# Optimization experiments

Hardware: AMD Instinct MI355X
Metric: run time of the kernel (lower is better)

Reference implementation:

```python
import jax, jax.numpy as jnp
import numpy as np


def _ln(x, w, b):
    m = x.mean(-1, keepdims=True)
    v = ((x - m) ** 2).mean(-1, keepdims=True)
    return (x - m) * jax.lax.rsqrt(v + 1e-5) * w + b


def _l2n(x):
    return x / jnp.clip(jnp.linalg.norm(x, axis=-1, keepdims=True), 1e-12, None)


def _forward(tokens, emb, ln1_w, ln1_b, wq, wkv, wo, wo_b, knn_scale,
             ln2_w, ln2_b, ff_w1, ff_b1, ff_w2, ff_b2, lnf_w, lnf_b,
             w_logits, b_logits, xl_mems, db_kv, knn_layer, topk):
    B, N = tokens.shape
    depth = wq.shape[0]
    H = knn_scale.shape[0]
    Dh = wkv.shape[-1] // 2
    XL = xl_mems.shape[2]
    NEG = jnp.finfo(emb.dtype).max
    x = emb[tokens]  # [B,N,dim]
    # causal mask with XL-cache offset: triu(j - i + 1)
    causal = jnp.triu(jnp.ones((N, N + XL), bool), XL + 1)
    for l in range(depth):
        h = _ln(x, ln1_w[l], ln1_b[l])
        q = (h @ wq[l]).reshape(B, N, H, Dh).transpose(0, 2, 1, 3)  # [B,H,N,Dh]
        kv = h @ wkv[l]
        k, v = kv[..., :Dh], kv[..., Dh:]  # single shared kv head [B,N,Dh]
        is_knn = (l == knn_layer)
        if is_knn:
            q, k = _l2n(q), _l2n(k)
            scale = jnp.exp(knn_scale)[None, :, None, None]
        else:
            q = q * (Dh ** -0.5)
            scale = 1.0
        k = jnp.concatenate((xl_mems[l, :, :, 0], k), axis=1)  # [B,N+XL,Dh]
        v = jnp.concatenate((xl_mems[l, :, :, 1], v), axis=1)
        sim = jnp.einsum('bhid,bjd->bhij', q, k) * scale
        sim = jnp.where(causal, -NEG, sim)
        if is_knn:
            dbk = _l2n(db_kv[..., 0, :])  # [B,M,Dh] stored keys are l2-normalized
            dbv = db_kv[..., 1, :]
            simdb = jnp.einsum('bhid,bmd->bhim', q, dbk)
            _, idx = jax.lax.top_k(simdb, topk)  # [B,H,N,topk] inner-product KNN
            mem_k = jax.vmap(lambda t, i: t[i])(dbk, idx)  # [B,H,N,topk,Dh]
            mem_v = jax.vmap(lambda t, i: t[i])(dbv, idx)
            sim_mem = jnp.einsum('bhid,bhijd->bhij', q, mem_k) * scale
            attn = jax.nn.softmax(jnp.concatenate((sim_mem, sim), axis=-1), axis=-1)
            mem_attn, loc_attn = attn[..., :topk], attn[..., topk:]
            out = (jnp.einsum('bhij,bjd->bhid', loc_attn, v)
                   + jnp.einsum('bhij,bhijd->bhid', mem_attn, mem_v))
        else:
            attn = jax.nn.softmax(sim, axis=-1)
            out = jnp.einsum('bhij,bjd->bhid', attn, v)
        out = out.transpose(0, 2, 1, 3).reshape(B, N, H * Dh)
        x = out @ wo[l] + wo_b[l] + x
        h = _ln(x, ln2_w[l], ln2_b[l])
        x = jax.nn.gelu(h @ ff_w1[l] + ff_b1[l], approximate=False) @ ff_w2[l] + ff_b2[l] + x
    return _ln(x, lnf_w, lnf_b) @ w_logits + b_logits


def setup_inputs() -> dict:
    B, N, DIM, H, DH, DEPTH, V, XL, M = 2, 1024, 1024, 16, 64, 4, 32000, 256, 4096
    key = jax.random.key(0)
    ks = jax.random.split(key, 12)
    s = 0.02
    rn = lambda k, sh: (jax.random.normal(k, sh) * s).astype(jnp.float32)
    return dict(
        tokens=jax.random.randint(ks[0], (B, N), 0, V, dtype=jnp.int32),
        emb=rn(ks[1], (V, DIM)),
        ln1_w=jnp.ones((DEPTH, DIM), jnp.float32), ln1_b=jnp.zeros((DEPTH, DIM), jnp.float32),
        wq=rn(ks[2], (DEPTH, DIM, H * DH)),
        wkv=rn(ks[3], (DEPTH, DIM, 2 * DH)),
        wo=rn(ks[4], (DEPTH, H * DH, DIM)), wo_b=jnp.zeros((DEPTH, DIM), jnp.float32),
        knn_scale=jnp.full((H,), float(np.log(20.0)), jnp.float32),
        ln2_w=jnp.ones((DEPTH, DIM), jnp.float32), ln2_b=jnp.zeros((DEPTH, DIM), jnp.float32),
        ff_w1=rn(ks[5], (DEPTH, DIM, 4 * DIM)), ff_b1=jnp.zeros((DEPTH, 4 * DIM), jnp.float32),
        ff_w2=rn(ks[6], (DEPTH, 4 * DIM, DIM)), ff_b2=jnp.zeros((DEPTH, DIM), jnp.float32),
        lnf_w=jnp.ones((DIM,), jnp.float32), lnf_b=jnp.zeros((DIM,), jnp.float32),
        w_logits=rn(ks[7], (DIM, V)), b_logits=jnp.zeros((V,), jnp.float32),
        xl_mems=jax.random.normal(ks[8], (DEPTH, B, XL, 2, DH), jnp.float32),
        db_kv=jax.random.normal(ks[9], (B, M, 2, DH), jnp.float32),
        knn_layer=2, topk=32,
    )


def reference(tokens, emb, ln1_w, ln1_b, wq, wkv, wo, wo_b, knn_scale,
              ln2_w, ln2_b, ff_w1, ff_b1, ff_w2, ff_b2, lnf_w, lnf_b,
              w_logits, b_logits, xl_mems, db_kv, knn_layer, topk):
    return _forward(tokens, emb, ln1_w, ln1_b, wq, wkv, wo, wo_b, knn_scale,
                    ln2_w, ln2_b, ff_w1, ff_b1, ff_w2, ff_b2, lnf_w, lnf_b,
                    w_logits, b_logits, xl_mems, db_kv, knn_layer, topk)
```

## Files before the change

### kernel.cpp

```cpp
#include <hip/hip_runtime.h>
#include <hip/hip_bf16.h>
#include <math.h>

#define BB 2
#define NSEQ 1024
#define DIM 1024
#define NH 16
#define DH 64
#define DEPTH 4
#define VOCAB 32000
#define XLM 256
#define MDB 4096
#define TOPK 32
#define KNN_LAYER 2
#define BNROWS (BB * NSEQ)
#define LOGITS_CHUNK 6400
#define NKEYS 1280
#define NQKV 1152
#define KSP_PS ((size_t)BB * NKEYS * DH)

typedef __bf16 bf16x8v __attribute__((ext_vector_type(8)));
typedef float f32x4v __attribute__((ext_vector_type(4)));
typedef unsigned short u16x8v __attribute__((ext_vector_type(8)));

__device__ __forceinline__ float bfbits2f(unsigned short u) {
    union { float f; unsigned int i; } v; v.i = ((unsigned int)u) << 16; return v.f;
}
__device__ __forceinline__ unsigned short f2bfbits(float f) {
    union { __hip_bfloat16 b; unsigned short u; } v;
    v.b = __float2bfloat16(f);
    return v.u;
}
__device__ __forceinline__ float bf2f(__hip_bfloat16 h) { return __bfloat162float(h); }
__device__ __forceinline__ __hip_bfloat16 f2bf(float f) { return __float2bfloat16(f); }

__device__ __forceinline__ void gload16(const void* gp, void* lp) {
    __builtin_amdgcn_global_load_lds(
        (const __attribute__((address_space(1))) unsigned int*)gp,
        (__attribute__((address_space(3))) unsigned int*)lp, 16, 0, 0);
}

__global__ __launch_bounds__(256) void embed_kernel(const int* __restrict__ tok,
                                                    const float* __restrict__ emb,
                                                    float* __restrict__ x) {
    int r = blockIdx.x, t = threadIdx.x;
    int id = tok[r];
    const float* er = emb + (size_t)id * DIM;
    float* xr = x + (size_t)r * DIM;
#pragma unroll
    for (int i = 0; i < 4; i++) xr[t + 256 * i] = er[t + 256 * i];
}

__global__ __launch_bounds__(256) void ln_kernel(const float* __restrict__ x,
                                                 const float* __restrict__ w,
                                                 const float* __restrict__ b,
                                                 __hip_bfloat16* __restrict__ y,
                                                 size_t ypS) {
    __shared__ float red[256];
    int r = blockIdx.x, t = threadIdx.x;
    const float* xr = x + (size_t)r * DIM;
    float v[4];
#pragma unroll
    for (int i = 0; i < 4; i++) v[i] = xr[t + 256 * i];
    float s = v[0] + v[1] + v[2] + v[3];
    red[t] = s; __syncthreads();
    for (int st = 128; st; st >>= 1) { if (t < st) red[t] += red[t + st]; __syncthreads(); }
    float mean = red[0] * (1.0f / DIM);
    __syncthreads();
    float s2 = 0.f;
#pragma unroll
    for (int i = 0; i < 4; i++) { float d = v[i] - mean; s2 += d * d; }
    red[t] = s2; __syncthreads();
    for (int st = 128; st; st >>= 1) { if (t < st) red[t] += red[t + st]; __syncthreads(); }
    float rs = rsqrtf(red[0] * (1.0f / DIM) + 1e-5f);
    __hip_bfloat16* yr = y + (size_t)r * DIM;
#pragma unroll
    for (int i = 0; i < 4; i++) {
        int c = t + 256 * i;
        float val = (v[i] - mean) * rs * w[c] + b[c];
        __hip_bfloat16 hv = f2bf(val);
        yr[c] = hv;
        yr[c + ypS] = f2bf(val - bf2f(hv));
    }
}

template <int NP>
__global__ __launch_bounds__(256) void combine_ln(const float* __restrict__ pbuf, size_t pS,
                                                  const float* __restrict__ bias,
                                                  float* __restrict__ x,
                                                  const float* __restrict__ w,
                                                  const float* __restrict__ b,
                                                  __hip_bfloat16* __restrict__ y,
                                                  size_t ypS) {
    __shared__ float red[256];
    int r = blockIdx.x, t = threadIdx.x;
    float v[4];
#pragma unroll
    for (int i = 0; i < 4; i++) {
        int c = t + 256 * i;
        size_t idx = (size_t)r * DIM + c;
        float s = bias[c] + x[idx];
#pragma unroll
        for (int z = 0; z < NP; z++) s += pbuf[(size_t)z * pS + idx];
        v[i] = s;
        x[idx] = s;
    }
    float s = v[0] + v[1] + v[2] + v[3];
    red[t] = s; __syncthreads();
    for (int st = 128; st; st >>= 1) { if (t < st) red[t] += red[t + st]; __syncthreads(); }
    float mean = red[0] * (1.0f / DIM);
    __syncthreads();
    float s2 = 0.f;
#pragma unroll
    for (int i = 0; i < 4; i++) { float d = v[i] - mean; s2 += d * d; }
    red[t] = s2; __syncthreads();
    for (int st = 128; st; st >>= 1) { if (t < st) red[t] += red[t + st]; __syncthreads(); }
    float rs = rsqrtf(red[0] * (1.0f / DIM) + 1e-5f);
    __hip_bfloat16* yr = y + (size_t)r * DIM;
#pragma unroll
    for (int i = 0; i < 4; i++) {
        int c = t + 256 * i;
        float val = (v[i] - mean) * rs * w[c] + b[c];
        __hip_bfloat16 hv = f2bf(val);
        yr[c] = hv;
        yr[c + ypS] = f2bf(val - bf2f(hv));
    }
}

__global__ void l2split_q(float* __restrict__ qf, unsigned short* __restrict__ qs,
                          size_t pS) {
    int r = blockIdx.x, t = threadIdx.x;
    size_t idx = (size_t)r * DH + t;
    float v = qf[idx];
    float s = v * v;
#pragma unroll
    for (int off = 32; off; off >>= 1) s += __shfl_xor(s, off, 64);
    float n = fmaxf(sqrtf(s), 1e-12f);
    v /= n;
    qf[idx] = v;
    unsigned short hv = f2bfbits(v);
    qs[idx] = hv;
    qs[idx + pS] = f2bfbits(v - bfbits2f(hv));
}

__global__ void dbnorm_kernel(const float* __restrict__ db, float* __restrict__ dbkn) {
    int r = blockIdx.x, t = threadIdx.x;
    float v = db[((size_t)r * 2 + 0) * DH + t];
    float s = v * v;
#pragma unroll
    for (int off = 32; off; off >>= 1) s += __shfl_xor(s, off, 64);
    float n = fmaxf(sqrtf(s), 1e-12f);
    dbkn[(size_t)r * DH + t] = v / n;
}

__global__ __launch_bounds__(256) void split_conv(const float* __restrict__ x,
                                                  unsigned short* __restrict__ y,
                                                  size_t pS, size_t n4) {
    size_t idx = (size_t)blockIdx.x * 256 + threadIdx.x;
    if (idx >= n4) return;
    float4 v = *(const float4*)&x[idx * 4];
    float vv[4] = {v.x, v.y, v.z, v.w};
    ushort4 h4, l4;
    unsigned short* hp = (unsigned short*)&h4;
    unsigned short* lp = (unsigned short*)&l4;
#pragma unroll
    for (int j = 0; j < 4; j++) {
        hp[j] = f2bfbits(vv[j]);
        lp[j] = f2bfbits(vv[j] - bfbits2f(hp[j]));
    }
    *(ushort4*)&y[idx * 4] = h4;
    *(ushort4*)&y[idx * 4 + pS] = l4;
}

template <int NP>
__global__ __launch_bounds__(256) void combine_k(const float* __restrict__ pbuf, size_t pS,
                                                 float* __restrict__ out,
                                                 const float* __restrict__ bias,
                                                 const float* __restrict__ res,
                                                 int N, size_t n4) {
    size_t idx = (size_t)blockIdx.x * 256 + threadIdx.x;
    if (idx >= n4) return;
    f32x4v s = *(const f32x4v*)&pbuf[idx * 4];
#pragma unroll
    for (int z = 1; z < NP; z++) {
        f32x4v v = *(const f32x4v*)&pbuf[(size_t)z * pS + idx * 4];
        s += v;
    }
    if (bias) {
        int col = (int)((idx * 4) % (size_t)N);
        const f32x4v bv = *(const f32x4v*)&bias[col];
        s += bv;
    }
    if (res) {
        f32x4v r = *(const f32x4v*)&res[idx * 4];
        s += r;
    }
    *(f32x4v*)&out[idx * 4] = s;
}

template <int NP>
__global__ __launch_bounds__(256) void combine_qkv(const float* __restrict__ pbuf, size_t pS,
                                                   float* __restrict__ qf,
                                                   float* __restrict__ kvf,
                                                   size_t n4) {
    size_t idx = (size_t)blockIdx.x * 256 + threadIdx.x;
    if (idx >= n4) return;
    f32x4v s = *(const f32x4v*)&pbuf[idx * 4];
#pragma unroll
    for (int z = 1; z < NP; z++) {
        f32x4v v = *(const f32x4v*)&pbuf[(size_t)z * pS + idx * 4];
        s += v;
    }
    size_t e = idx * 4;
    size_t row = e / NQKV;
    int col = (int)(e - row * NQKV);
    if (col < DIM) *(f32x4v*)&qf[row * DIM + col] = s;
    else *(f32x4v*)&kvf[row * 128 + (col - DIM)] = s;
}

template <int NP>
__global__ __launch_bounds__(256) void combine_gelu_split(const float* __restrict__ pbuf, size_t pS,
                                                          const float* __restrict__ bias, int N,
                                                          unsigned short* __restrict__ y, size_t ypS,
                                                          size_t n4) {
    size_t idx = (size_t)blockIdx.x * 256 + threadIdx.x;
    if (idx >= n4) return;
    f32x4v s = *(const f32x4v*)&pbuf[idx * 4];
#pragma unroll
    for (int z = 1; z < NP; z++) {
        f32x4v v = *(const f32x4v*)&pbuf[(size_t)z * pS + idx * 4];
        s += v;
    }
    int col = (int)((idx * 4) % (size_t)N);
    const f32x4v bv = *(const f32x4v*)&bias[col];
    s += bv;
    ushort4 h4, l4;
    unsigned short* hp = (unsigned short*)&h4;
    unsigned short* lp = (unsigned short*)&l4;
#pragma unroll
    for (int j = 0; j < 4; j++) {
        float v = s[j];
        v = 0.5f * v * (1.0f + erff(v * 0.70710678118654752f));
        hp[j] = f2bfbits(v);
        lp[j] = f2bfbits(v - bfbits2f(hp[j]));
    }
    *(ushort4*)&y[idx * 4] = h4;
    *(ushort4*)&y[idx * 4 + ypS] = l4;
}

template <int NORM>
__global__ void kv_prep(const float* __restrict__ kvf, const float* __restrict__ xlm,
                        unsigned short* __restrict__ ksp, unsigned short* __restrict__ vtp) {
    int key = blockIdx.x, b = blockIdx.y, d = threadIdx.x;
    float kvv, vvv;
    if (key < XLM) {
        kvv = xlm[(((size_t)b * XLM + key) * 2 + 0) * DH + d];
        vvv = xlm[(((size_t)b * XLM + key) * 2 + 1) * DH + d];
    } else {
        const float* r = &kvf[(size_t)(b * NSEQ + key - XLM) * 128];
        kvv = r[d]; vvv = r[64 + d];
        if (NORM) {
            float s = kvv * kvv;
#pragma unroll
            for (int off = 32; off; off >>= 1) s += __shfl_xor(s, off, 64);
            kvv /= fmaxf(sqrtf(s), 1e-12f);
        }
    }
    unsigned short kh = f2bfbits(kvv), kl = f2bfbits(kvv - bfbits2f(kh));
    unsigned short vh = f2bfbits(vvv), vl = f2bfbits(vvv - bfbits2f(vh));
    size_t ko = (size_t)b * NKEYS * DH + (size_t)key * DH + d;
    ksp[ko] = kh; ksp[ko + KSP_PS] = kl;
    size_t vo = (size_t)b * DH * NKEYS + (size_t)d * NKEYS + key;
    vtp[vo] = vh; vtp[vo + KSP_PS] = vl;
}

__global__ __launch_bounds__(256) void wconv(const float* __restrict__ W,
                                             __hip_bfloat16* __restrict__ WT,
                                             size_t wpS, int K, int N, int ldw,
                                             int wlo) {
    __shared__ float tile[64][65];
    int k0 = blockIdx.x * 64, n0 = blockIdx.y * 64;
    int t = threadIdx.x;
    int r = t >> 4, c4 = (t & 15) * 4;
#pragma unroll
    for (int rr = 0; rr < 4; rr++) {
        int row = rr * 16 + r;
        float4 v = *(const float4*)&W[(size_t)(k0 + row) * ldw + n0 + c4];
        tile[row][c4] = v.x; tile[row][c4 + 1] = v.y; tile[row][c4 + 2] = v.z; tile[row][c4 + 3] = v.w;
    }
    __syncthreads();
#pragma unroll
    for (int rr = 0; rr < 4; rr++) {
        int nrow = rr * 16 + r;
        size_t base = (size_t)(n0 + nrow) * K + k0 + c4;
#pragma unroll
        for (int j = 0; j < 4; j++) {
            float val = tile[c4 + j][nrow];
            __hip_bfloat16 hv = f2bf(val);
            WT[base + j] = hv;
            if (wlo) WT[base + j + wpS] = f2bf(val - bf2f(hv));
        }
    }
}

template <typename OT, int ACT, int TERMS, int MODE>
__global__ __launch_bounds__(256) void gemm_split(const __hip_bfloat16* __restrict__ A, int lda, size_t apS,
                                                  const __hip_bfloat16* __restrict__ BT, int ldb, size_t bpS,
                                                  OT* __restrict__ C, int ldc, size_t cpS, int K,
                                                  const float* __restrict__ bias,
                                                  const float* __restrict__ res,
                                                  int bh0) {
    __shared__ __align__(16) __hip_bfloat16 sAh[128 * 32];
    __shared__ __align__(16) __hip_bfloat16 sBh[128 * 32];
    __shared__ __align__(16) __hip_bfloat16 sAl[TERMS >= 2 ? 128 * 32 : 1];
    __shared__ __align__(16) __hip_bfloat16 sBl[TERMS >= 3 ? 128 * 32 : 1];
    if constexpr (MODE == 1) {
        int bh = bh0 + blockIdx.z;
        A += ((size_t)(bh >> 4) * NSEQ) * lda + (bh & 15) * DH;
        BT += (size_t)(bh >> 4) * MDB * ldb;
        C += (size_t)blockIdx.z * NSEQ * ldc;
    }
    if constexpr (MODE == 2) {
        A += (size_t)blockIdx.z * K;
        BT += (size_t)blockIdx.z * K;
        C += (size_t)blockIdx.z * cpS;
    }
    int bn = blockIdx.x * 128;
    int bm = blockIdx.y * 128;
    int t = threadIdx.x;
    int lane = t & 63, wid = t >> 6;
    int wr = wid >> 1, wc = wid & 1;
    int lr = lane & 15, kc = lane >> 4;

    f32x4v acc[4][4];
#pragma unroll
    for (int m = 0; m < 4; m++)
#pragma unroll
        for (int n = 0; n < 4; n++) acc[m][n] = (f32x4v){0.f, 0.f, 0.f, 0.f};

    for (int k0 = 0; k0 < K; k0 += 32) {
        __syncthreads();
#pragma unroll
        for (int it = 0; it < 2; it++) {
            int e = wid * 128 + it * 64 + lane;
            int r = e >> 2;
            int cl = (e & 3) ^ ((r >> 1) & 3);
            size_t aoff = (size_t)(bm + r) * lda + k0 + cl * 8;
            size_t boff = (size_t)(bn + r) * ldb + k0 + cl * 8;
            int dst = (wid * 128 + it * 64) * 8;
            gload16(&A[aoff], &sAh[dst]);
            gload16(&BT[boff], &sBh[dst]);
            if constexpr (TERMS >= 2) gload16(&A[aoff + apS], &sAl[dst]);
            if constexpr (TERMS >= 3) gload16(&BT[boff + bpS], &sBl[dst]);
        }
        __syncthreads();

        bf16x8v ah[4], al[4], bh[4], bl[4];
#pragma unroll
        for (int m = 0; m < 4; m++) {
            int row = wr * 64 + m * 16 + lr;
            int off = row * 32 + ((kc ^ ((row >> 1) & 3)) << 3);
            ah[m] = *(const bf16x8v*)&sAh[off];
            if constexpr (TERMS >= 2) al[m] = *(const bf16x8v*)&sAl[off];
        }
#pragma unroll
        for (int n = 0; n < 4; n++) {
            int row = wc * 64 + n * 16 + lr;
            int off = row * 32 + ((kc ^ ((row >> 1) & 3)) << 3);
            bh[n] = *(const bf16x8v*)&sBh[off];
            if constexpr (TERMS >= 3) bl[n] = *(const bf16x8v*)&sBl[off];
        }
#pragma unroll
        for (int m = 0; m < 4; m++)
#pragma unroll
            for (int n = 0; n < 4; n++) {
                acc[m][n] = __builtin_amdgcn_mfma_f32_16x16x32_bf16(ah[m], bh[n], acc[m][n], 0, 0, 0);
                if constexpr (TERMS >= 2)
                    acc[m][n] = __builtin_amdgcn_mfma_f32_16x16x32_bf16(al[m], bh[n], acc[m][n], 0, 0, 0);
                if constexpr (TERMS >= 3)
                    acc[m][n] = __builtin_amdgcn_mfma_f32_16x16x32_bf16(ah[m], bl[n], acc[m][n], 0, 0, 0);
            }
    }

#pragma unroll
    for (int m = 0; m < 4; m++) {
#pragma unroll
        for (int n = 0; n < 4; n++) {
            int gcol = bn + wc * 64 + n * 16 + lr;
            float bv = bias ? bias[gcol] : 0.f;
#pragma unroll
            for (int j = 0; j < 4; j++) {
                int grow = bm + wr * 64 + m * 16 + kc * 4 + j;
                float v = acc[m][n][j] + bv;
                if (ACT == 1) v = 0.5f * v * (1.0f + erff(v * 0.70710678118654752f));
                if (res) v += res[(size_t)grow * ldc + gcol];
                size_t idx = (size_t)grow * ldc + gcol;
                if constexpr (__is_same(OT, float)) {
                    C[idx] = v;
                } else if constexpr (__is_same(OT, unsigned short)) {
                    C[idx] = f2bfbits(v);
                } else {
                    __hip_bfloat16 hv = f2bf(v);
                    C[idx] = hv;
                    C[idx + cpS] = f2bf(v - bf2f(hv));
                }
            }
        }
    }
}

template <int KNNL>
__global__ __launch_bounds__(256) void flash_kernel(const float* __restrict__ q,
                                                    const unsigned short* __restrict__ ksp,
                                                    const unsigned short* __restrict__ vtp,
                                                    const float* __restrict__ knn_scale,
                                                    __hip_bfloat16* __restrict__ out,
                                                    size_t opS,
                                                    float* __restrict__ stats) {
    __shared__ __align__(16) unsigned short sKh[2][4096];
    __shared__ __align__(16) unsigned short sKl[2][4096];
    __shared__ __align__(16) unsigned short sVh[2][4096];
    __shared__ __align__(16) unsigned short sVl[2][4096];
    __shared__ __align__(16) float sPf[4 * 16 * 64];

    int qt = blockIdx.x, h = blockIdx.y, b = blockIdx.z;
    int q0 = qt * 64;
    int t = threadIdx.x;
    int w = t >> 6;
    int lane = t & 63;
    int lr = lane & 15, kc = lane >> 4;
    int wbase = w * 1024;

    float scale = KNNL ? __expf(knn_scale[h]) : 0.125f;

    bf16x8v qh[2], ql[2];
    {
        const float* qbase = q + (size_t)(b * NSEQ + q0 + w * 16 + lr) * DIM + h * DH;
#pragma unroll
        for (int ks = 0; ks < 2; ks++) {
            const float* s = qbase + ks * 32 + kc * 8;
            float4 a = *(const float4*)s;
            float4 c2 = *(const float4*)(s + 4);
            float vv[8] = {a.x, a.y, a.z, a.w, c2.x, c2.y, c2.z, c2.w};
            u16x8v hi, lo;
#pragma unroll
            for (int j = 0; j < 8; j++) {
                hi[j] = f2bfbits(vv[j]);
                lo[j] = f2bfbits(vv[j] - bfbits2f(hi[j]));
            }
            qh[ks] = *(bf16x8v*)&hi;
            ql[ks] = *(bf16x8v*)&lo;
        }
    }

    float m[4], l[4];
    f32x4v o[4];
#pragma unroll
    for (int j = 0; j < 4; j++) { m[j] = -1e30f; l[j] = 0.f; }
#pragma unroll
    for (int f = 0; f < 4; f++) o[f] = (f32x4v){0.f, 0.f, 0.f, 0.f};

    int ntiles = 5 + qt;
    size_t kbase = (size_t)b * NKEYS * DH;
    size_t vbase = (size_t)b * DH * NKEYS;

    auto stage = [&](int buf, int T) {
#pragma unroll
        for (int i2 = 0; i2 < 2; i2++) {
            int cbase = i2 * 256 + w * 64;
            int c = cbase + lane;
            int key = c >> 3, ch = (c & 7) ^ (key & 7);
            size_t ko = kbase + (size_t)(T * 64 + key) * DH + ch * 8;
            gload16(&ksp[ko], &sKh[buf][cbase * 8]);
            gload16(&ksp[ko + KSP_PS], &sKl[buf][cbase * 8]);
            int dim = c >> 3, k8 = (c & 7) ^ (dim & 7);
            size_t vo = vbase + (size_t)dim * NKEYS + T * 64 + k8 * 8;
            gload16(&vtp[vo], &sVh[buf][cbase * 8]);
            gload16(&vtp[vo + KSP_PS], &sVl[buf][cbase * 8]);
        }
    };

    stage(0, 0);
    __syncthreads();
    int cur = 0;

    for (int T = 0; T < ntiles; T++) {
        if (T + 1 < ntiles) stage(cur ^ 1, T + 1);

        f32x4v s4[4];
#pragma unroll
        for (int n = 0; n < 4; n++) s4[n] = (f32x4v){0.f, 0.f, 0.f, 0.f};
#pragma unroll
        for (int ks = 0; ks < 2; ks++) {
            bf16x8v qh_ = qh[ks], ql_ = ql[ks];
#pragma unroll
            for (int n = 0; n < 4; n++) {
                int row = n * 16 + lr;
                int off = row * 64 + (((ks * 4 + kc) ^ (lr & 7)) << 3);
                bf16x8v kh = *(const bf16x8v*)&sKh[cur][off];
                bf16x8v kl = *(const bf16x8v*)&sKl[cur][off];
                s4[n] = __builtin_amdgcn_mfma_f32_16x16x32_bf16(qh_, kh, s4[n], 0, 0, 0);
                s4[n] = __builtin_amdgcn_mfma_f32_16x16x32_bf16(ql_, kh, s4[n], 0, 0, 0);
                s4[n] = __builtin_amdgcn_mfma_f32_16x16x32_bf16(qh_, kl, s4[n], 0, 0, 0);
            }
        }

#pragma unroll
        for (int n = 0; n < 4; n++) {
            int key = T * 64 + n * 16 + lr;
#pragma unroll
            for (int j = 0; j < 4; j++) {
                int gq = q0 + w * 16 + kc * 4 + j;
                float sv = s4[n][j] * scale;
                s4[n][j] = (key <= XLM + gq) ? sv : -1e30f;
            }
        }

        float tm[4];
#pragma unroll
        for (int j = 0; j < 4; j++) {
            float v = fmaxf(fmaxf(s4[0][j], s4[1][j]), fmaxf(s4[2][j], s4[3][j]));
            v = fmaxf(v, __shfl_xor(v, 1, 64));
            v = fmaxf(v, __shfl_xor(v, 2, 64));
            v = fmaxf(v, __shfl_xor(v, 4, 64));
            v = fmaxf(v, __shfl_xor(v, 8, 64));
            tm[j] = v;
        }
        float alpha[4];
#pragma unroll
        for (int j = 0; j < 4; j++) {
            float mnew = fmaxf(m[j], tm[j]);
            alpha[j] = __expf(m[j] - mnew);
            m[j] = mnew;
        }
        float psum[4] = {0.f, 0.f, 0.f, 0.f};
#pragma unroll
        for (int n = 0; n < 4; n++)
#pragma unroll
            for (int j = 0; j < 4; j++) {
                float p = __expf(s4[n][j] - m[j]);
                s4[n][j] = p;
                psum[j] += p;
            }
#pragma unroll
        for (int j = 0; j < 4; j++) {
            float v = psum[j];
            v += __shfl_xor(v, 1, 64);
            v += __shfl_xor(v, 2, 64);
            v += __shfl_xor(v, 4, 64);
            v += __shfl_xor(v, 8, 64);
            l[j] = l[j] * alpha[j] + v;
        }
#pragma unroll
        for (int f = 0; f < 4; f++)
#pragma unroll
            for (int j = 0; j < 4; j++) o[f][j] *= alpha[j];

#pragma unroll
        for (int n = 0; n < 4; n++) {
            int chunkcol = 2 * n + (lr >> 3);
#pragma unroll
            for (int j = 0; j < 4; j++) {
                int row = kc * 4 + j;
                int off = wbase + row * 64 + (((chunkcol ^ (row & 7)) << 3) + (lr & 7));
                sPf[off] = s4[n][j];
            }
        }

#pragma unroll
        for (int ks = 0; ks < 2; ks++) {
            int poff = wbase + lr * 64 + (((ks * 4 + kc) ^ (lr & 7)) << 3);
            float4 a = *(const float4*)&sPf[poff];
            float4 c2 = *(const float4*)&sPf[poff + 4];
            float vv[8] = {a.x, a.y, a.z, a.w, c2.x, c2.y, c2.z, c2.w};
            u16x8v hib, lob;
#pragma unroll
            for (int j = 0; j < 8; j++) {
                hib[j] = f2bfbits(vv[j]);
                lob[j] = f2bfbits(vv[j] - bfbits2f(hib[j]));
            }
            bf16x8v ph = *(bf16x8v*)&hib;
            bf16x8v pl = *(bf16x8v*)&lob;
#pragma unroll
            for (int f = 0; f < 4; f++) {
                int row = f * 16 + lr;
                int off = row * 64 + (((ks * 4 + kc) ^ (lr & 7)) << 3);
                bf16x8v vh = *(const bf16x8v*)&sVh[cur][off];
                bf16x8v vl = *(const bf16x8v*)&sVl[cur][off];
                o[f] = __builtin_amdgcn_mfma_f32_16x16x32_bf16(ph, vh, o[f], 0, 0, 0);
                o[f] = __builtin_amdgcn_mfma_f32_16x16x32_bf16(pl, vh, o[f], 0, 0, 0);
                o[f] = __builtin_amdgcn_mfma_f32_16x16x32_bf16(ph, vl, o[f], 0, 0, 0);
            }
        }

        __syncthreads();
        cur ^= 1;
    }

    float inv[4];
#pragma unroll
    for (int j = 0; j < 4; j++) inv[j] = 1.0f / l[j];
    unsigned short* outu = (unsigned short*)out;
#pragma unroll
    for (int f = 0; f < 4; f++)
#pragma unroll
        for (int j = 0; j < 4; j++) {
            int gq = q0 + w * 16 + kc * 4 + j;
            size_t oidx = (size_t)(b * NSEQ + gq) * DIM + h * DH + f * 16 + lr;
            float v = o[f][j] * inv[j];
            unsigned short hv = f2bfbits(v);
            outu[oidx] = hv;
            outu[oidx + opS] = f2bfbits(v - bfbits2f(hv));
        }
    if (KNNL && lr == 0) {
#pragma unroll
        for (int j = 0; j < 4; j++) {
            int gq = q0 + w * 16 + kc * 4 + j;
            size_t srow = (((size_t)b * NH + h) * NSEQ + gq) * 2;
            stats[srow] = m[j];
            stats[srow + 1] = l[j];
        }
    }
}

__global__ __launch_bounds__(256) void knn_select(const unsigned short* __restrict__ simdb,
                                                  const float* __restrict__ db,
                                                  const float* __restrict__ qf,
                                                  const float* __restrict__ dbkn,
                                                  const float* __restrict__ knn_scale,
                                                  const float* __restrict__ stats,
                                                  __hip_bfloat16* __restrict__ out,
                                                  size_t opS,
                                                  int bh0) {
    __shared__ unsigned short sv[4 * 4096];

    int bh = bh0 + blockIdx.y;
    int b = bh >> 4, h = bh & 15;
    int t = threadIdx.x;
    int w = t >> 6, lane = t & 63;
    int i = blockIdx.x * 4 + w;
    unsigned short* svw = &sv[w * 4096];

    const unsigned short* srow = &simdb[((size_t)blockIdx.y * NSEQ + i) * MDB];
#pragma unroll
    for (int it = 0; it < 8; it++) {
        int g = it * 64 + lane;
        int c = g >> 3, sub = g & 7;
        u16x8v d = *(const u16x8v*)&srow[(size_t)g * 8];
        *(u16x8v*)&svw[c * 64 + ((sub ^ (c & 7)) << 3)] = d;
    }

    float lmax = -1e30f; int lidx = 0;
#pragma unroll
    for (int c = 0; c < 64; c++) {
        float v = bfbits2f(svw[c * 64 + (lane ^ ((c & 7) << 3))]);
        if (v > lmax) { lmax = v; lidx = c * 64 + lane; }
    }

    int tidx = 0;
    for (int it = 0; it < TOPK; it++) {
        float v = lmax; int idx = lidx;
#pragma unroll
        for (int off = 32; off; off >>= 1) {
            float v2 = __shfl_xor(v, off, 64);
            int i2 = __shfl_xor(idx, off, 64);
            if (v2 > v || (v2 == v && i2 < idx)) { v = v2; idx = i2; }
        }
        if (lane == it) tidx = idx;
        int col = idx & 63, cc = idx >> 6;
        if (lane == 0) svw[cc * 64 + (col ^ ((cc & 7) << 3))] = 0xFF80;
        float rv = bfbits2f(svw[lane * 64 + (col ^ ((lane & 7) << 3))]);
        int ridx = lane * 64 + col;
#pragma unroll
        for (int off = 32; off; off >>= 1) {
            float v2 = __shfl_xor(rv, off, 64);
            int i2 = __shfl_xor(ridx, off, 64);
            if (v2 > rv || (v2 == rv && i2 < ridx)) { rv = v2; ridx = i2; }
        }
        if (lane == col) { lmax = rv; lidx = ridx; }
    }

    float srec = -1e30f;
    if (lane < TOPK) {
        const float* qrow = &qf[(size_t)(b * NSEQ + i) * DIM + h * DH];
        const float* krow = &dbkn[((size_t)b * MDB + tidx) * DH];
        float s = 0.f;
#pragma unroll
        for (int d4 = 0; d4 < 16; d4++) {
            float4 a = *(const float4*)&qrow[d4 * 4];
            float4 k2 = *(const float4*)&krow[d4 * 4];
            s += a.x * k2.x + a.y * k2.y + a.z * k2.z + a.w * k2.w;
        }
        srec = s;
    }

    float scl = __expf(knn_scale[h]);
    size_t srow_idx = (((size_t)b * NH + h) * NSEQ + i) * 2;
    float m_loc = stats[srow_idx], l_loc = stats[srow_idx + 1];
    float mm = srec;
#pragma unroll
    for (int off = 32; off; off >>= 1) mm = fmaxf(mm, __shfl_xor(mm, off, 64));
    float M = fmaxf(m_loc, mm * scl);
    float co = __expf(m_loc - M);
    float e = (lane < TOPK) ? __expf(srec * scl - M) : 0.f;
    float esum = e;
#pragma unroll
    for (int off = 32; off; off >>= 1) esum += __shfl_xor(esum, off, 64);
    float denom = l_loc * co + esum;

    float acc = 0.f;
#pragma unroll
    for (int j = 0; j < TOPK; j++) {
        int idxj = __shfl(tidx, j, 64);
        float ej = __shfl(e, j, 64);
        acc += ej * db[(((size_t)b * MDB + idxj) * 2 + 1) * DH + lane];
    }

    size_t op = (size_t)(b * NSEQ + i) * DIM + h * DH + lane;
    float o_loc = bf2f(out[op]) + bf2f(out[op + opS]);
    float nv = (o_loc * l_loc * co + acc) / denom;
    __hip_bfloat16 hv = f2bf(nv);
    out[op] = hv;
    out[op + opS] = f2bf(nv - bf2f(hv));
}

extern "C" void kernel_launch(void* const* d_in, const int* in_sizes, int n_in,
                              void* d_out, int out_size, void* d_ws, size_t ws_size,
                              hipStream_t stream) {
    const int* tokens = (const int*)d_in[0];
    const float* emb = (const float*)d_in[1];
    const float* ln1_w = (const float*)d_in[2];
    const float* ln1_b = (const float*)d_in[3];
    const float* wq = (const float*)d_in[4];
    const float* wkv = (const float*)d_in[5];
    const float* wo = (const float*)d_in[6];
    const float* wo_b = (const float*)d_in[7];
    const float* knn_scale = (const float*)d_in[8];
    const float* ln2_w = (const float*)d_in[9];
    const float* ln2_b = (const float*)d_in[10];
    const float* ff_w1 = (const float*)d_in[11];
    const float* ff_b1 = (const float*)d_in[12];
    const float* ff_w2 = (const float*)d_in[13];
    const float* ff_b2 = (const float*)d_in[14];
    const float* lnf_w = (const float*)d_in[15];
    const float* lnf_b = (const float*)d_in[16];
    const float* w_logits = (const float*)d_in[17];
    const float* b_logits = (const float*)d_in[18];
    const float* xl_mems = (const float*)d_in[19];
    const float* db_kv = (const float*)d_in[20];

    const size_t PS_H = (size_t)BNROWS * DIM;
    char* p = (char*)d_ws;
    float* x = (float*)p;                p += PS_H * 4;
    __hip_bfloat16* hb = (__hip_bfloat16*)p;  p += PS_H * 2 * 2;
    float* qf = (float*)p;               p += PS_H * 4;
    float* kvf = (float*)p;              p += (size_t)BNROWS * 128 * 4;
    float* dbkn = (float*)p;             p += (size_t)BB * MDB * DH * 4;
    float* stats = (float*)p;            p += (size_t)BB * NH * NSEQ * 2 * 4;
    unsigned short* ksp = (unsigned short*)p; p += KSP_PS * 2 * 2;
    unsigned short* vtp = (unsigned short*)p; p += KSP_PS * 2 * 2;
    __hip_bfloat16* wT = (__hip_bfloat16*)p; p += (size_t)4096 * DIM * 2 * 2;

    unsigned short* qsplit = (unsigned short*)wT;
    unsigned short* dbks = (unsigned short*)wT + 2 * PS_H;
    const size_t PS_DB = (size_t)BB * MDB * DH;

    const size_t PS_MID = (size_t)BNROWS * 4 * DIM;
    __hip_bfloat16* midb = (__hip_bfloat16*)d_out;
    float* logits = (float*)d_out;
    float* part = (float*)((char*)d_out + ((size_t)96 << 20));

    const size_t PS_QKV = (size_t)BNROWS * NQKV;

    embed_kernel<<<BNROWS, 256, 0, stream>>>(tokens, emb, x);
    dbnorm_kernel<<<BB * MDB, 64, 0, stream>>>(db_kv, dbkn);
    ln_kernel<<<BNROWS, 256, 0, stream>>>(x, ln1_w, ln1_b, hb, PS_H);

    for (int l = 0; l < DEPTH; l++) {
        const float* wq_l = wq + (size_t)l * DIM * DIM;
        const float* wkv_l = wkv + (size_t)l * DIM * 128;
        const float* wo_l = wo + (size_t)l * DIM * DIM;
        const float* xlm_l = xl_mems + (size_t)l * BB * XLM * 2 * DH;

        wconv<<<dim3(16, 16), 256, 0, stream>>>(wq_l, wT, (size_t)NQKV * DIM, DIM, DIM, DIM, 1);
        wconv<<<dim3(16, 2), 256, 0, stream>>>(wkv_l, wT + (size_t)DIM * DIM, (size_t)NQKV * DIM, DIM, 128, 128, 1);
        gemm_split<float, 0, 3, 2><<<dim3(NQKV / 128, BNROWS / 128, 4), 256, 0, stream>>>(
            hb, DIM, PS_H, wT, DIM, (size_t)NQKV * DIM, part, NQKV, PS_QKV, 256, nullptr, nullptr, 0);
        combine_qkv<4><<<(PS_QKV / 4 + 255) / 256, 256, 0, stream>>>(
            part, PS_QKV, qf, kvf, PS_QKV / 4);

        if (l == KNN_LAYER) {
            l2split_q<<<BNROWS * NH, 64, 0, stream>>>(qf, qsplit, PS_H);
            kv_prep<1><<<dim3(NKEYS, BB), 64, 0, stream>>>(kvf, xlm_l, ksp, vtp);
            split_conv<<<(PS_DB / 4 + 255) / 256, 256, 0, stream>>>(dbkn, dbks, PS_DB, PS_DB / 4);
            flash_kernel<1><<<dim3(NSEQ / 64, NH, BB), 256, 0, stream>>>(
                qf, ksp, vtp, knn_scale, hb, PS_H, stats);
            const int CHUNK = 8;
            for (int bh0 = 0; bh0 < BB * NH; bh0 += CHUNK) {
                gemm_split<unsigned short, 0, 1, 1><<<dim3(MDB / 128, NSEQ / 128, CHUNK), 256, 0, stream>>>(
                    (const __hip_bfloat16*)qsplit, DIM, PS_H,
                    (const __hip_bfloat16*)dbks, DH, PS_DB,
                    (unsigned short*)d_out, MDB, 0, DH, nullptr, nullptr, bh0);
                knn_select<<<dim3(NSEQ / 4, CHUNK), 256, 0, stream>>>(
                    (const unsigned short*)d_out, db_kv, qf, dbkn, knn_scale, stats, hb, PS_H, bh0);
            }
        } else {
            kv_prep<0><<<dim3(NKEYS, BB), 64, 0, stream>>>(kvf, xlm_l, ksp, vtp);
            flash_kernel<0><<<dim3(NSEQ / 64, NH, BB), 256, 0, stream>>>(
                qf, ksp, vtp, knn_scale, hb, PS_H, stats);
        }

        wconv<<<dim3(16, 16), 256, 0, stream>>>(wo_l, wT, (size_t)DIM * DIM, DIM, DIM, DIM, 1);
        gemm_split<float, 0, 3, 2><<<dim3(DIM / 128, BNROWS / 128, 4), 256, 0, stream>>>(
            hb, DIM, PS_H, wT, DIM, (size_t)DIM * DIM, part, DIM, PS_H, 256, nullptr, nullptr, 0);
        combine_ln<4><<<BNROWS, 256, 0, stream>>>(
            part, PS_H, wo_b + (size_t)l * DIM, x,
            ln2_w + (size_t)l * DIM, ln2_b + (size_t)l * DIM, hb, PS_H);

        wconv<<<dim3(16, 64), 256, 0, stream>>>(ff_w1 + (size_t)l * DIM * 4 * DIM, wT, (size_t)4096 * DIM, DIM, 4 * DIM, 4 * DIM, 1);
        gemm_split<float, 0, 3, 2><<<dim3(4 * DIM / 128, BNROWS / 128, 2), 256, 0, stream>>>(
            hb, DIM, PS_H, wT, DIM, (size_t)4096 * DIM, part, 4 * DIM, PS_MID, 512, nullptr, nullptr, 0);
        combine_gelu_split<2><<<(PS_MID / 4 + 255) / 256, 256, 0, stream>>>(
            part, PS_MID, ff_b1 + (size_t)l * 4 * DIM, 4 * DIM,
            (unsigned short*)midb, PS_MID, PS_MID / 4);

        wconv<<<dim3(64, 16), 256, 0, stream>>>(ff_w2 + (size_t)l * 4 * DIM * DIM, wT, (size_t)DIM * 4096, 4 * DIM, DIM, DIM, 1);
        gemm_split<float, 0, 3, 2><<<dim3(DIM / 128, BNROWS / 128, 4), 256, 0, stream>>>(
            midb, 4 * DIM, PS_MID, wT, 4 * DIM, (size_t)DIM * 4096, part, DIM, PS_H, 1024, nullptr, nullptr, 0);
        const float* nw = (l < DEPTH - 1) ? ln1_w + (size_t)(l + 1) * DIM : lnf_w;
        const float* nb = (l < DEPTH - 1) ? ln1_b + (size_t)(l + 1) * DIM : lnf_b;
        combine_ln<4><<<BNROWS, 256, 0, stream>>>(
            part, PS_H, ff_b2 + (size_t)l * DIM, x, nw, nb, hb, PS_H);
    }

    for (int c0 = 0; c0 < VOCAB; c0 += LOGITS_CHUNK) {
        wconv<<<dim3(16, LOGITS_CHUNK / 64), 256, 0, stream>>>(
            w_logits + c0, wT, 0, DIM, LOGITS_CHUNK, VOCAB, 0);
        gemm_split<float, 0, 1, 0><<<dim3(LOGITS_CHUNK / 128, BNROWS / 128), 256, 0, stream>>>(
            hb, DIM, PS_H, wT, DIM, 0, logits + c0, VOCAB, 0, DIM,
            b_logits + c0, nullptr, 0);
    }
}
```

Before: 2.229 ms.

## Fuse db normalization with bf16 split, pack row kernels, swizzle GEMM block order

Merges the database-key L2 normalization and the hi/lo bf16 split into one kernel. That kernel now runs inside the KNN layer instead of at startup, which removes one pass over the normalized keys. The per-row l2 kernels now pack four 64-wide rows into each 256-thread block to cut block count and launch overhead. The GEMM remaps block IDs into eight interleaved groups, presumably to improve L2 or cache locality across workgroups. The unused combine_k template is also deleted.

```diff
diff --git a/kernel.cpp b/kernel.cpp
--- a/kernel.cpp
+++ b/kernel.cpp
@@ -127,10 +127,13 @@
     }
 }
 
-__global__ void l2split_q(float* __restrict__ qf, unsigned short* __restrict__ qs,
-                          size_t pS) {
-    int r = blockIdx.x, t = threadIdx.x;
-    size_t idx = (size_t)r * DH + t;
+__global__ __launch_bounds__(256) void l2split_q(float* __restrict__ qf,
+                                                 unsigned short* __restrict__ qs,
+                                                 size_t pS) {
+    int t = threadIdx.x;
+    int w = t >> 6, lane = t & 63;
+    int r = blockIdx.x * 4 + w;
+    size_t idx = (size_t)r * DH + lane;
     float v = qf[idx];
     float s = v * v;
 #pragma unroll
@@ -143,59 +146,24 @@
     qs[idx + pS] = f2bfbits(v - bfbits2f(hv));
 }
 
-__global__ void dbnorm_kernel(const float* __restrict__ db, float* __restrict__ dbkn) {
-    int r = blockIdx.x, t = threadIdx.x;
-    float v = db[((size_t)r * 2 + 0) * DH + t];
+__global__ __launch_bounds__(256) void dbprep(const float* __restrict__ db,
+                                              float* __restrict__ dbkn,
+                                              unsigned short* __restrict__ dbks,
+                                              size_t pS) {
+    int t = threadIdx.x;
+    int w = t >> 6, lane = t & 63;
+    int r = blockIdx.x * 4 + w;
+    float v = db[((size_t)r * 2 + 0) * DH + lane];
     float s = v * v;
 #pragma unroll
     for (int off = 32; off; off >>= 1) s += __shfl_xor(s, off, 64);
     float n = fmaxf(sqrtf(s), 1e-12f);
-    dbkn[(size_t)r * DH + t] = v / n;
-}
-
-__global__ __launch_bounds__(256) void split_conv(const float* __restrict__ x,
-                                                  unsigned short* __restrict__ y,
-                                                  size_t pS, size_t n4) {
-    size_t idx = (size_t)blockIdx.x * 256 + threadIdx.x;
-    if (idx >= n4) return;
-    float4 v = *(const float4*)&x[idx * 4];
-    float vv[4] = {v.x, v.y, v.z, v.w};
-    ushort4 h4, l4;
-    unsigned short* hp = (unsigned short*)&h4;
-    unsigned short* lp = (unsigned short*)&l4;
-#pragma unroll
-    for (int j = 0; j < 4; j++) {
-        hp[j] = f2bfbits(vv[j]);
-        lp[j] = f2bfbits(vv[j] - bfbits2f(hp[j]));
-    }
-    *(ushort4*)&y[idx * 4] = h4;
-    *(ushort4*)&y[idx * 4 + pS] = l4;
-}
-
-template <int NP>
-__global__ __launch_bounds__(256) void combine_k(const float* __restrict__ pbuf, size_t pS,
-                                                 float* __restrict__ out,
-                                                 const float* __restrict__ bias,
-                                                 const float* __restrict__ res,
-                                                 int N, size_t n4) {
-    size_t idx = (size_t)blockIdx.x * 256 + threadIdx.x;
-    if (idx >= n4) return;
-    f32x4v s = *(const f32x4v*)&pbuf[idx * 4];
-#pragma unroll
-    for (int z = 1; z < NP; z++) {
-        f32x4v v = *(const f32x4v*)&pbuf[(size_t)z * pS + idx * 4];
-        s += v;
-    }
-    if (bias) {
-        int col = (int)((idx * 4) % (size_t)N);
-        const f32x4v bv = *(const f32x4v*)&bias[col];
-        s += bv;
-    }
-    if (res) {
-        f32x4v r = *(const f32x4v*)&res[idx * 4];
-        s += r;
-    }
-    *(f32x4v*)&out[idx * 4] = s;
+    v /= n;
+    size_t idx = (size_t)r * DH + lane;
+    dbkn[idx] = v;
+    unsigned short hv = f2bfbits(v);
+    dbks[idx] = hv;
+    dbks[idx + pS] = f2bfbits(v - bfbits2f(hv));
 }
 
 template <int NP>
@@ -325,8 +293,14 @@
         BT += (size_t)blockIdx.z * K;
         C += (size_t)blockIdx.z * cpS;
     }
-    int bn = blockIdx.x * 128;
-    int bm = blockIdx.y * 128;
+    int nwg = gridDim.x * gridDim.y;
+    int bid = blockIdx.y * gridDim.x + blockIdx.x;
+    if ((nwg & 7) == 0) {
+        int cpx = nwg >> 3;
+        bid = (bid & 7) * cpx + (bid >> 3);
+    }
+    int bn = (bid % gridDim.x) * 128;
+    int bm = (bid / gridDim.x) * 128;
     int t = threadIdx.x;
     int lane = t & 63, wid = t >> 6;
     int wr = wid >> 1, wc = wid & 1;
@@ -773,7 +747,6 @@
     const size_t PS_QKV = (size_t)BNROWS * NQKV;
 
     embed_kernel<<<BNROWS, 256, 0, stream>>>(tokens, emb, x);
-    dbnorm_kernel<<<BB * MDB, 64, 0, stream>>>(db_kv, dbkn);
     ln_kernel<<<BNROWS, 256, 0, stream>>>(x, ln1_w, ln1_b, hb, PS_H);
 
     for (int l = 0; l < DEPTH; l++) {
@@ -790,9 +763,9 @@
             part, PS_QKV, qf, kvf, PS_QKV / 4);
 
         if (l == KNN_LAYER) {
-            l2split_q<<<BNROWS * NH, 64, 0, stream>>>(qf, qsplit, PS_H);
+            l2split_q<<<BNROWS * NH / 4, 256, 0, stream>>>(qf, qsplit, PS_H);
             kv_prep<1><<<dim3(NKEYS, BB), 64, 0, stream>>>(kvf, xlm_l, ksp, vtp);
-            split_conv<<<(PS_DB / 4 + 255) / 256, 256, 0, stream>>>(dbkn, dbks, PS_DB, PS_DB / 4);
+            dbprep<<<BB * MDB / 4, 256, 0, stream>>>(db_kv, dbkn, dbks, PS_DB);
             flash_kernel<1><<<dim3(NSEQ / 64, NH, BB), 256, 0, stream>>>(
                 qf, ksp, vtp, knn_scale, hb, PS_H, stats);
             const int CHUNK = 8;
```

New measurement: 2.227 ms. No clear change (-0.1%).
